# Kernel optimization log

Measured on AMD Instinct MI355X. Metric: run time of the kernel, lower is better.

## Reference

```python
import jax, jax.numpy as jnp
import numpy as np

H = 64

def _ln(x, g, b, eps=1e-5):
    m = x.mean(-1, keepdims=True)
    v = ((x - m) ** 2).mean(-1, keepdims=True)
    return (x - m) * jax.lax.rsqrt(v + eps) * g + b

def _sage(x_src, x_dst, src, dst, Wl, bl, Wr, n_dst):
    # PyG SAGEConv: mean-aggregate neighbors, lin_l(agg) + lin_r(x_dst)
    msg = x_src[src]  # [E, H] gather
    s = jax.ops.segment_sum(msg, dst, num_segments=n_dst)
    cnt = jax.ops.segment_sum(jnp.ones((src.shape[0], 1), x_src.dtype), dst, num_segments=n_dst)
    mean = s / jnp.maximum(cnt, 1.0)
    return mean @ Wl + bl + x_dst @ Wr

def _hetero_conv(xn, xc, edge_sim, men_src, men_dst, edge_rel, Wl, bl, Wr):
    # relation order: 0=similar_to (news->news), 1=mentions (news->company), 2=related_to (company->company)
    Nn, Nc = xn.shape[0], xc.shape[0]
    on = _sage(xn, xn, edge_sim[0], edge_sim[1], Wl[0], bl[0], Wr[0], Nn)
    oc = (_sage(xn, xc, men_src, men_dst, Wl[1], bl[1], Wr[1], Nc)
          + _sage(xc, xc, edge_rel[0], edge_rel[1], Wl[2], bl[2], Wr[2], Nc))  # HeteroConv aggr='sum'
    return on, oc

def setup_inputs():
    key = jax.random.key(0)
    ks = jax.random.split(key, 16)
    Nn, Nc = 100000, 5000
    Es, Em, Er = 3200000, 1000000, 160000
    init = lambda k, s: (jax.random.normal(k, s, jnp.float32) * 0.05)
    d = {}
    d['x_news'] = jax.random.normal(ks[0], (Nn, 385), jnp.float32)
    d['x_company'] = jax.random.normal(ks[1], (Nc, 24), jnp.float32)
    d['edge_sim'] = jax.random.randint(ks[2], (2, Es), 0, Nn)
    d['men_src'] = jax.random.randint(ks[3], (Em,), 0, Nn)
    d['men_dst'] = jax.random.randint(ks[4], (Em,), 0, Nc)
    d['edge_rel'] = jax.random.randint(ks[5], (2, Er), 0, Nc)
    d['nw_W'] = init(ks[6], (385, H)); d['nw_b'] = jnp.zeros((H,), jnp.float32)
    d['cw_W'] = init(ks[7], (24, H)); d['cw_b'] = jnp.zeros((H,), jnp.float32)
    d['n1n_g'] = jnp.ones((H,), jnp.float32); d['n1n_b'] = jnp.zeros((H,), jnp.float32)
    d['n1c_g'] = jnp.ones((H,), jnp.float32); d['n1c_b'] = jnp.zeros((H,), jnp.float32)
    d['c1_Wl'] = init(ks[8], (3, H, H)); d['c1_bl'] = jnp.zeros((3, H), jnp.float32)
    d['c1_Wr'] = init(ks[9], (3, H, H))
    d['c2_Wl'] = init(ks[10], (3, H, H)); d['c2_bl'] = jnp.zeros((3, H), jnp.float32)
    d['c2_Wr'] = init(ks[11], (3, H, H))
    d['cls_W1'] = init(ks[12], (H, 32)); d['cls_b1'] = jnp.zeros((32,), jnp.float32)
    d['cls_W2'] = init(ks[13], (32, 1)); d['cls_b2'] = jnp.zeros((1,), jnp.float32)
    return d

def reference(x_news, x_company, edge_sim, men_src, men_dst, edge_rel,
              nw_W, nw_b, cw_W, cw_b, n1n_g, n1n_b, n1c_g, n1c_b,
              c1_Wl, c1_bl, c1_Wr, c2_Wl, c2_bl, c2_Wr,
              cls_W1, cls_b1, cls_W2, cls_b2):
    xn0 = jax.nn.relu(x_news @ nw_W + nw_b)
    xc0 = jax.nn.relu(x_company @ cw_W + cw_b)
    on, oc = _hetero_conv(xn0, xc0, edge_sim, men_src, men_dst, edge_rel, c1_Wl, c1_bl, c1_Wr)
    xn = _ln(jax.nn.relu(on), n1n_g, n1n_b)
    xc = _ln(jax.nn.relu(oc + xc0), n1c_g, n1c_b)
    # dropout is identity in eval mode
    on2, oc2 = _hetero_conv(xn, xc, edge_sim, men_src, men_dst, edge_rel, c2_Wl, c2_bl, c2_Wr)
    comp = jax.nn.relu(oc2 + xc)  # [Nc, H]
    h = jax.nn.relu(comp @ cls_W1 + cls_b1)
    return (h @ cls_W2 + cls_b2).squeeze(-1)  # [Nc]
```

## Files before the change

### kernel.cpp

```cpp
#include <hip/hip_runtime.h>
#include <hip/hip_bf16.h>

#define HF 64

__global__ __launch_bounds__(256) void k_proj_news(
    const float* __restrict__ A, const float* __restrict__ W,
    const float* __restrict__ b, float* __restrict__ out, int M)
{
    __shared__ float As[16][68];
    __shared__ float Ws[16][64];
    const int t = threadIdx.x;
    const int r0 = blockIdx.x * 64;
    const int rt = t >> 4, ct = t & 15;
    float acc[4][4] = {};

    for (int c0 = 0; c0 < 385; c0 += 16) {
        int lr = t >> 2, lk0 = (t & 3) * 4;
        #pragma unroll
        for (int j = 0; j < 4; ++j) {
            int k = c0 + lk0 + j;
            float v = 0.f;
            if ((r0 + lr) < M && k < 385) v = A[(size_t)(r0 + lr) * 385 + k];
            As[lk0 + j][lr] = v;
        }
        #pragma unroll
        for (int j = 0; j < 4; ++j) {
            int idx = j * 256 + t;
            int k = idx >> 6, col = idx & 63;
            float v = 0.f;
            if (c0 + k < 385) v = W[(size_t)(c0 + k) * 64 + col];
            Ws[k][col] = v;
        }
        __syncthreads();
        #pragma unroll
        for (int kk = 0; kk < 16; ++kk) {
            float4 a = *(const float4*)&As[kk][rt * 4];
            float4 w = *(const float4*)&Ws[kk][ct * 4];
            float av[4] = {a.x, a.y, a.z, a.w};
            float wv[4] = {w.x, w.y, w.z, w.w};
            #pragma unroll
            for (int i = 0; i < 4; ++i)
                #pragma unroll
                for (int j = 0; j < 4; ++j)
                    acc[i][j] += av[i] * wv[j];
        }
        __syncthreads();
    }
    float4 bv = *(const float4*)&b[ct * 4];
    float bb[4] = {bv.x, bv.y, bv.z, bv.w};
    #pragma unroll
    for (int i = 0; i < 4; ++i) {
        int row = r0 + rt * 4 + i;
        if (row < M) {
            float4 o;
            o.x = fmaxf(acc[i][0] + bb[0], 0.f);
            o.y = fmaxf(acc[i][1] + bb[1], 0.f);
            o.z = fmaxf(acc[i][2] + bb[2], 0.f);
            o.w = fmaxf(acc[i][3] + bb[3], 0.f);
            *(float4*)&out[(size_t)row * HF + ct * 4] = o;
        }
    }
}

__global__ __launch_bounds__(256) void k_proj_comp(
    const float* __restrict__ A, const float* __restrict__ W,
    const float* __restrict__ b, float* __restrict__ out, int M)
{
    int idx = blockIdx.x * blockDim.x + threadIdx.x;
    if (idx >= M * HF) return;
    int row = idx >> 6, col = idx & 63;
    float acc = b[col];
    #pragma unroll
    for (int k = 0; k < 24; ++k)
        acc += A[(size_t)row * 24 + k] * W[k * HF + col];
    out[idx] = fmaxf(acc, 0.f);
}

__global__ void k_count(const int* __restrict__ dst, int n, int base,
                        unsigned* __restrict__ cnt)
{
    for (int i = blockIdx.x * blockDim.x + threadIdx.x; i < n;
         i += gridDim.x * blockDim.x)
        atomicAdd(&cnt[base + dst[i]], 1u);
}

__global__ __launch_bounds__(1024) void k_scan(
    const unsigned* __restrict__ cnt, int n,
    int* __restrict__ off, int* __restrict__ cursor)
{
    __shared__ int wsum[17];
    __shared__ int carry_s;
    if (threadIdx.x == 0) carry_s = 0;
    __syncthreads();
    const int lane = threadIdx.x & 63, wid = threadIdx.x >> 6;
    for (int base = 0; base < n; base += 1024) {
        int i = base + (int)threadIdx.x;
        int v = (i < n) ? (int)cnt[i] : 0;
        int x = v;
        #pragma unroll
        for (int s = 1; s < 64; s <<= 1) {
            int t = __shfl_up(x, s, 64);
            if (lane >= s) x += t;
        }
        if (lane == 63) wsum[wid] = x;
        __syncthreads();
        if (threadIdx.x == 0) {
            int run = 0;
            #pragma unroll
            for (int w = 0; w < 16; ++w) { int t = wsum[w]; wsum[w] = run; run += t; }
            wsum[16] = run;
        }
        __syncthreads();
        int excl = x - v + wsum[wid] + carry_s;
        if (i < n) { off[i] = excl; cursor[i] = excl; }
        __syncthreads();
        if (threadIdx.x == 0) carry_s += wsum[16];
        __syncthreads();
    }
    if (threadIdx.x == 0) off[n] = carry_s;
}

__global__ void k_fill(const int* __restrict__ src, const int* __restrict__ dst,
                       int n, int dbase, int* __restrict__ cursor,
                       int* __restrict__ bucket)
{
    for (int i = blockIdx.x * blockDim.x + threadIdx.x; i < n;
         i += gridDim.x * blockDim.x) {
        int pos = atomicAdd(&cursor[dbase + dst[i]], 1);
        bucket[pos] = src[i];
    }
}

__global__ __launch_bounds__(256) void k_gather(
    const int* __restrict__ off, const int* __restrict__ bucket,
    const float* __restrict__ x, float* __restrict__ out, int obase, int M)
{
    const int lane = threadIdx.x & 63;
    const int w = (int)((blockIdx.x * blockDim.x + threadIdx.x) >> 6);
    if (w >= M) return;
    int o0 = off[obase + w], o1 = off[obase + w + 1];
    float a0 = 0.f, a1 = 0.f, a2 = 0.f, a3 = 0.f;
    int e = o0;
    for (; e + 4 <= o1; e += 4) {
        int s0 = bucket[e], s1 = bucket[e + 1], s2 = bucket[e + 2], s3 = bucket[e + 3];
        a0 += x[(size_t)s0 * HF + lane];
        a1 += x[(size_t)s1 * HF + lane];
        a2 += x[(size_t)s2 * HF + lane];
        a3 += x[(size_t)s3 * HF + lane];
    }
    for (; e < o1; ++e) a0 += x[(size_t)bucket[e] * HF + lane];
    float acc = (a0 + a1) + (a2 + a3);
    float inv = 1.f / fmaxf((float)(o1 - o0), 1.f);
    out[(size_t)w * HF + lane] = acc * inv;
}

__global__ __launch_bounds__(256) void k_news_l1(
    const float* __restrict__ mean_sim, const float* __restrict__ xn0,
    const float* __restrict__ Wl, const float* __restrict__ bl,
    const float* __restrict__ Wr,
    const float* __restrict__ g, const float* __restrict__ be,
    float* __restrict__ xn, int M)
{
    __shared__ float A1[64][68];
    __shared__ float A2[64][68];
    const int t = threadIdx.x;
    const int r0 = blockIdx.x * 64;
    const int lrow = t & 63;
    const int wq = t >> 6;

    bool rok = (r0 + lrow) < M;
    #pragma unroll
    for (int j4 = 0; j4 < 4; ++j4) {
        int k0 = wq * 16 + j4 * 4;
        float4 v1 = make_float4(0.f, 0.f, 0.f, 0.f), v2 = v1;
        if (rok) {
            v1 = *(const float4*)&mean_sim[(size_t)(r0 + lrow) * HF + k0];
            v2 = *(const float4*)&xn0[(size_t)(r0 + lrow) * HF + k0];
        }
        A1[k0 + 0][lrow] = v1.x; A1[k0 + 1][lrow] = v1.y;
        A1[k0 + 2][lrow] = v1.z; A1[k0 + 3][lrow] = v1.w;
        A2[k0 + 0][lrow] = v2.x; A2[k0 + 1][lrow] = v2.y;
        A2[k0 + 2][lrow] = v2.z; A2[k0 + 3][lrow] = v2.w;
    }
    __syncthreads();

    const int rt = t >> 4, ct = t & 15;
    float acc[4][4] = {};
    #pragma unroll 16
    for (int kk = 0; kk < 64; ++kk) {
        float4 a1 = *(const float4*)&A1[kk][rt * 4];
        float4 a2 = *(const float4*)&A2[kk][rt * 4];
        float4 wl = *(const float4*)&Wl[(size_t)kk * HF + ct * 4];
        float4 wr = *(const float4*)&Wr[(size_t)kk * HF + ct * 4];
        float a1v[4] = {a1.x, a1.y, a1.z, a1.w};
        float a2v[4] = {a2.x, a2.y, a2.z, a2.w};
        float wlv[4] = {wl.x, wl.y, wl.z, wl.w};
        float wrv[4] = {wr.x, wr.y, wr.z, wr.w};
        #pragma unroll
        for (int i = 0; i < 4; ++i)
            #pragma unroll
            for (int j = 0; j < 4; ++j)
                acc[i][j] += a1v[i] * wlv[j] + a2v[i] * wrv[j];
    }
    __syncthreads();
    float (*C)[68] = A1;
    float4 blv = *(const float4*)&bl[ct * 4];
    float blb[4] = {blv.x, blv.y, blv.z, blv.w};
    #pragma unroll
    for (int i = 0; i < 4; ++i) {
        float4 o;
        o.x = fmaxf(acc[i][0] + blb[0], 0.f);
        o.y = fmaxf(acc[i][1] + blb[1], 0.f);
        o.z = fmaxf(acc[i][2] + blb[2], 0.f);
        o.w = fmaxf(acc[i][3] + blb[3], 0.f);
        *(float4*)&C[rt * 4 + i][ct * 4] = o;
    }
    __syncthreads();

    const int lane = t & 63, wid = t >> 6;
    float gl = g[lane], bel = be[lane];
    for (int rr = 0; rr < 16; ++rr) {
        int row = wid * 16 + rr;
        float v = C[row][lane];
        float s = v, q = v * v;
        #pragma unroll
        for (int m = 1; m < 64; m <<= 1) {
            s += __shfl_xor(s, m, 64);
            q += __shfl_xor(q, m, 64);
        }
        float mean = s * (1.f / 64.f);
        float var = q * (1.f / 64.f) - mean * mean;
        float r = rsqrtf(var + 1e-5f);
        int grow = r0 + row;
        if (grow < M) xn[(size_t)grow * HF + lane] = (v - mean) * r * gl + bel;
    }
}

__global__ __launch_bounds__(256) void k_comp_l1(
    const float* __restrict__ mean_men, const float* __restrict__ mean_rel,
    const float* __restrict__ xc0,
    const float* __restrict__ Wl1, const float* __restrict__ bl1,
    const float* __restrict__ Wr1,
    const float* __restrict__ Wl2, const float* __restrict__ bl2,
    const float* __restrict__ Wr2,
    const float* __restrict__ g, const float* __restrict__ be,
    float* __restrict__ xc, int M)
{
    const int lane = threadIdx.x & 63;
    const int node = (int)((blockIdx.x * blockDim.x + threadIdx.x) >> 6);
    if (node >= M) return;
    float mm = mean_men[(size_t)node * HF + lane];
    float mr = mean_rel[(size_t)node * HF + lane];
    float xv = xc0[(size_t)node * HF + lane];
    float acc = bl1[lane] + bl2[lane];
    #pragma unroll 8
    for (int k = 0; k < 64; ++k) {
        float amm = __shfl(mm, k, 64);
        float amr = __shfl(mr, k, 64);
        float ax  = __shfl(xv, k, 64);
        acc += amm * Wl1[k * HF + lane] + ax * Wr1[k * HF + lane]
             + amr * Wl2[k * HF + lane] + ax * Wr2[k * HF + lane];
    }
    float pre = fmaxf(acc + xv, 0.f);
    float s = pre, q = pre * pre;
    #pragma unroll
    for (int m = 1; m < 64; m <<= 1) {
        s += __shfl_xor(s, m, 64);
        q += __shfl_xor(q, m, 64);
    }
    float mean = s * (1.f / 64.f);
    float var = q * (1.f / 64.f) - mean * mean;
    float r = rsqrtf(var + 1e-5f);
    xc[(size_t)node * HF + lane] = (pre - mean) * r * g[lane] + be[lane];
}

__global__ __launch_bounds__(256) void k_final(
    const float* __restrict__ mean_men, const float* __restrict__ mean_rel,
    const float* __restrict__ xc,
    const float* __restrict__ Wl1, const float* __restrict__ bl1,
    const float* __restrict__ Wr1,
    const float* __restrict__ Wl2, const float* __restrict__ bl2,
    const float* __restrict__ Wr2,
    const float* __restrict__ W1, const float* __restrict__ b1,
    const float* __restrict__ W2, const float* __restrict__ b2,
    float* __restrict__ out, int M)
{
    const int lane = threadIdx.x & 63;
    const int node = (int)((blockIdx.x * blockDim.x + threadIdx.x) >> 6);
    if (node >= M) return;
    float mm = mean_men[(size_t)node * HF + lane];
    float mr = mean_rel[(size_t)node * HF + lane];
    float xv = xc[(size_t)node * HF + lane];
    float acc = bl1[lane] + bl2[lane];
    #pragma unroll 8
    for (int k = 0; k < 64; ++k) {
        float amm = __shfl(mm, k, 64);
        float amr = __shfl(mr, k, 64);
        float ax  = __shfl(xv, k, 64);
        acc += amm * Wl1[k * HF + lane] + ax * (Wr1[k * HF + lane] + Wr2[k * HF + lane])
             + amr * Wl2[k * HF + lane];
    }
    float comp = fmaxf(acc + xv, 0.f);
    const int l31 = lane & 31;
    float hacc = b1[l31];
    #pragma unroll 8
    for (int j = 0; j < 64; ++j) {
        float cj = __shfl(comp, j, 64);
        hacc += cj * W1[j * 32 + l31];
    }
    float h = fmaxf(hacc, 0.f);
    float p = (lane < 32) ? h * W2[l31] : 0.f;
    #pragma unroll
    for (int m = 16; m >= 1; m >>= 1) p += __shfl_xor(p, m, 64);
    if (lane == 0) out[node] = p + b2[0];
}

extern "C" void kernel_launch(void* const* d_in, const int* in_sizes, int n_in,
                              void* d_out, int out_size, void* d_ws, size_t ws_size,
                              hipStream_t stream)
{
    const float* x_news  = (const float*)d_in[0];
    const float* x_comp  = (const float*)d_in[1];
    const int*   edge_sim = (const int*)d_in[2];
    const int*   men_src  = (const int*)d_in[3];
    const int*   men_dst  = (const int*)d_in[4];
    const int*   edge_rel = (const int*)d_in[5];
    const float* nw_W = (const float*)d_in[6];
    const float* nw_b = (const float*)d_in[7];
    const float* cw_W = (const float*)d_in[8];
    const float* cw_b = (const float*)d_in[9];
    const float* n1n_g = (const float*)d_in[10];
    const float* n1n_b = (const float*)d_in[11];
    const float* n1c_g = (const float*)d_in[12];
    const float* n1c_b = (const float*)d_in[13];
    const float* c1_Wl = (const float*)d_in[14];
    const float* c1_bl = (const float*)d_in[15];
    const float* c1_Wr = (const float*)d_in[16];
    const float* c2_Wl = (const float*)d_in[17];
    const float* c2_bl = (const float*)d_in[18];
    const float* c2_Wr = (const float*)d_in[19];
    const float* cls_W1 = (const float*)d_in[20];
    const float* cls_b1 = (const float*)d_in[21];
    const float* cls_W2 = (const float*)d_in[22];
    const float* cls_b2 = (const float*)d_in[23];

    const int Nn = in_sizes[0] / 385;
    const int Nc = in_sizes[1] / 24;
    const int Es = in_sizes[2] / 2;
    const int Em = in_sizes[3];
    const int Er = in_sizes[5] / 2;
    const int* sim_src = edge_sim;
    const int* sim_dst = edge_sim + Es;
    const int* rel_src = edge_rel;
    const int* rel_dst = edge_rel + Er;
    const int ND = Nn + 2 * Nc;
    const int E  = Es + Em + Er;

    float* ws = (float*)d_ws;
    size_t o = 0;
    unsigned* cnt = (unsigned*)(ws + o); o += ND;
    int* off    = (int*)(ws + o); o += ND + 1;
    int* cursor = (int*)(ws + o); o += ND;
    int* bucket = (int*)(ws + o); o += E;
    float* mean_sim = ws + o; o += (size_t)Nn * HF;
    float* mean_men1 = ws + o; o += (size_t)Nc * HF;
    float* mean_rel1 = ws + o; o += (size_t)Nc * HF;
    float* xn0 = ws + o; o += (size_t)Nn * HF;
    float* xn  = ws + o; o += (size_t)Nn * HF;
    float* xc0 = ws + o; o += (size_t)Nc * HF;
    float* xc  = ws + o; o += (size_t)Nc * HF;
    float* mean_men2 = mean_sim;
    float* mean_rel2 = mean_sim + (size_t)Nc * HF;

    hipMemsetAsync(cnt, 0, (size_t)ND * sizeof(unsigned), stream);

    k_proj_news<<<(Nn + 63) / 64, 256, 0, stream>>>(x_news, nw_W, nw_b, xn0, Nn);
    k_proj_comp<<<(Nc * HF + 255) / 256, 256, 0, stream>>>(x_comp, cw_W, cw_b, xc0, Nc);

    k_count<<<1024, 256, 0, stream>>>(sim_dst, Es, 0, cnt);
    k_count<<<512, 256, 0, stream>>>(men_dst, Em, Nn, cnt);
    k_count<<<256, 256, 0, stream>>>(rel_dst, Er, Nn + Nc, cnt);
    k_scan<<<1, 1024, 0, stream>>>(cnt, ND, off, cursor);
    k_fill<<<1024, 256, 0, stream>>>(sim_src, sim_dst, Es, 0, cursor, bucket);
    k_fill<<<512, 256, 0, stream>>>(men_src, men_dst, Em, Nn, cursor, bucket);
    k_fill<<<256, 256, 0, stream>>>(rel_src, rel_dst, Er, Nn + Nc, cursor, bucket);

    k_gather<<<(Nn + 3) / 4, 256, 0, stream>>>(off, bucket, xn0, mean_sim, 0, Nn);
    k_gather<<<(Nc + 3) / 4, 256, 0, stream>>>(off, bucket, xn0, mean_men1, Nn, Nc);
    k_gather<<<(Nc + 3) / 4, 256, 0, stream>>>(off, bucket, xc0, mean_rel1, Nn + Nc, Nc);

    k_news_l1<<<(Nn + 63) / 64, 256, 0, stream>>>(
        mean_sim, xn0, c1_Wl, c1_bl, c1_Wr, n1n_g, n1n_b, xn, Nn);
    k_comp_l1<<<(Nc * HF + 255) / 256, 256, 0, stream>>>(
        mean_men1, mean_rel1, xc0,
        c1_Wl + 4096, c1_bl + 64, c1_Wr + 4096,
        c1_Wl + 8192, c1_bl + 128, c1_Wr + 8192,
        n1c_g, n1c_b, xc, Nc);

    k_gather<<<(Nc + 3) / 4, 256, 0, stream>>>(off, bucket, xn, mean_men2, Nn, Nc);
    k_gather<<<(Nc + 3) / 4, 256, 0, stream>>>(off, bucket, xc, mean_rel2, Nn + Nc, Nc);

    k_final<<<(Nc * HF + 255) / 256, 256, 0, stream>>>(
        mean_men2, mean_rel2, xc,
        c2_Wl + 4096, c2_bl + 64, c2_Wr + 4096,
        c2_Wl + 8192, c2_bl + 128, c2_Wr + 8192,
        cls_W1, cls_b1, cls_W2, cls_b2, (float*)d_out, Nc);
}
```

Baseline: 1.506 ms.

## Replace full CSR build for similar_to edges with coarse binning and LDS aggregation

For the 3.2M news->news edges, the per-destination CSR fill is replaced by a coarse partition into bins of 256 destinations. Each entry packs the source index with the low 8 bits of the destination. Each bin is then aggregated by one 512-thread block that accumulates rows in LDS with shared atomics. The aim is to cut the scattered global atomics and writes of the per-node fill and the uncoalesced gather pass. In exchange it adds a bin histogram and scan, needs 64KB of LDS per block, and packs source indices into 17 bits, which assumes fewer than 131072 news nodes.

```diff
diff --git a/kernel.cpp b/kernel.cpp
--- a/kernel.cpp
+++ b/kernel.cpp
@@ -2,6 +2,9 @@
 #include <hip/hip_bf16.h>
 
 #define HF 64
+#define BINSZ 256
+#define NBIN_S 392
+#define PCHUNK 4096
 
 __global__ __launch_bounds__(256) void k_proj_news(
     const float* __restrict__ A, const float* __restrict__ W,
@@ -84,6 +87,20 @@
         atomicAdd(&cnt[base + dst[i]], 1u);
 }
 
+__global__ __launch_bounds__(256) void k_binhist(
+    const int* __restrict__ dst, int n, unsigned* __restrict__ bins)
+{
+    __shared__ unsigned h[NBIN_S];
+    for (int i = threadIdx.x; i < NBIN_S; i += 256) h[i] = 0;
+    __syncthreads();
+    for (int i = blockIdx.x * blockDim.x + threadIdx.x; i < n;
+         i += gridDim.x * blockDim.x)
+        atomicAdd(&h[dst[i] >> 8], 1u);
+    __syncthreads();
+    for (int i = threadIdx.x; i < NBIN_S; i += 256)
+        if (h[i]) atomicAdd(&bins[i], h[i]);
+}
+
 __global__ __launch_bounds__(1024) void k_scan(
     const unsigned* __restrict__ cnt, int n,
     int* __restrict__ off, int* __restrict__ cursor)
@@ -118,6 +135,76 @@
         __syncthreads();
     }
     if (threadIdx.x == 0) off[n] = carry_s;
+}
+
+__global__ __launch_bounds__(256) void k_partition(
+    const int* __restrict__ src, const int* __restrict__ dst, int n,
+    int* __restrict__ cursor, unsigned* __restrict__ binned)
+{
+    __shared__ unsigned stage[PCHUNK];
+    __shared__ int hist[NBIN_S];
+    __shared__ int rank[NBIN_S];
+    __shared__ int base[NBIN_S];
+    for (long long c0 = (long long)blockIdx.x * PCHUNK; c0 < n;
+         c0 += (long long)gridDim.x * PCHUNK) {
+        int nc = min((long long)PCHUNK, (long long)n - c0);
+        for (int i = threadIdx.x; i < NBIN_S; i += 256) { hist[i] = 0; rank[i] = 0; }
+        __syncthreads();
+        for (int i = threadIdx.x; i < nc; i += 256) {
+            int d = dst[c0 + i];
+            stage[i] = (unsigned)src[c0 + i] | ((unsigned)(d & 255) << 17);
+            atomicAdd(&hist[d >> 8], 1);
+        }
+        __syncthreads();
+        for (int i = threadIdx.x; i < NBIN_S; i += 256)
+            if (hist[i]) base[i] = atomicAdd(&cursor[i], hist[i]);
+        __syncthreads();
+        for (int i = threadIdx.x; i < nc; i += 256) {
+            int b = dst[c0 + i] >> 8;
+            int r = atomicAdd(&rank[b], 1);
+            binned[base[b] + r] = stage[i];
+        }
+        __syncthreads();
+    }
+}
+
+__global__ __launch_bounds__(512) void k_binagg(
+    const unsigned* __restrict__ binned, const int* __restrict__ bin_off,
+    const unsigned* __restrict__ cnt, const float* __restrict__ feat,
+    float* __restrict__ out, int M)
+{
+    __shared__ __align__(16) float acc[BINSZ * HF];
+    const int tid = threadIdx.x, lane = tid & 63, wv = tid >> 6;
+    for (int i = tid; i < BINSZ * HF / 4; i += 512)
+        ((float4*)acc)[i] = make_float4(0.f, 0.f, 0.f, 0.f);
+    __syncthreads();
+    const int b = blockIdx.x;
+    const int e0 = bin_off[b], e1 = bin_off[b + 1];
+    for (int eb = e0 + wv * 4; eb < e1; eb += 32) {
+        unsigned p0 = 0, p1 = 0, p2 = 0, p3 = 0;
+        int m = e1 - eb;
+        p0 = binned[eb];
+        if (m > 1) p1 = binned[eb + 1];
+        if (m > 2) p2 = binned[eb + 2];
+        if (m > 3) p3 = binned[eb + 3];
+        float v0 = feat[(size_t)(p0 & 0x1FFFF) * HF + lane];
+        float v1 = (m > 1) ? feat[(size_t)(p1 & 0x1FFFF) * HF + lane] : 0.f;
+        float v2 = (m > 2) ? feat[(size_t)(p2 & 0x1FFFF) * HF + lane] : 0.f;
+        float v3 = (m > 3) ? feat[(size_t)(p3 & 0x1FFFF) * HF + lane] : 0.f;
+        atomicAdd(&acc[(p0 >> 17) * HF + lane], v0);
+        if (m > 1) atomicAdd(&acc[(p1 >> 17) * HF + lane], v1);
+        if (m > 2) atomicAdd(&acc[(p2 >> 17) * HF + lane], v2);
+        if (m > 3) atomicAdd(&acc[(p3 >> 17) * HF + lane], v3);
+    }
+    __syncthreads();
+    const int d0 = b * BINSZ;
+    for (int r = wv; r < BINSZ; r += 8) {
+        int row = d0 + r;
+        if (row < M) {
+            float inv = 1.f / fmaxf((float)cnt[row], 1.f);
+            out[(size_t)row * HF + lane] = acc[r * HF + lane] * inv;
+        }
+    }
 }
 
 __global__ void k_fill(const int* __restrict__ src, const int* __restrict__ dst,
@@ -353,16 +440,21 @@
     const int* sim_dst = edge_sim + Es;
     const int* rel_src = edge_rel;
     const int* rel_dst = edge_rel + Er;
-    const int ND = Nn + 2 * Nc;
-    const int E  = Es + Em + Er;
+    const int NDc = 2 * Nc;
 
     float* ws = (float*)d_ws;
     size_t o = 0;
-    unsigned* cnt = (unsigned*)(ws + o); o += ND;
-    int* off    = (int*)(ws + o); o += ND + 1;
-    int* cursor = (int*)(ws + o); o += ND;
-    int* bucket = (int*)(ws + o); o += E;
-    float* mean_sim = ws + o; o += (size_t)Nn * HF;
+    unsigned* cnt_sim = (unsigned*)(ws + o); o += Nn;
+    unsigned* cnt_c   = (unsigned*)(ws + o); o += NDc;
+    unsigned* binh    = (unsigned*)(ws + o); o += NBIN_S;
+    const size_t zero_bytes = o * sizeof(float);
+    int* bin_off = (int*)(ws + o); o += NBIN_S + 1;
+    int* bin_cur = (int*)(ws + o); o += NBIN_S;
+    int* off_c   = (int*)(ws + o); o += NDc + 1;
+    int* cur_c   = (int*)(ws + o); o += NDc;
+    unsigned* binned_sim = (unsigned*)(ws + o); o += Es;
+    int* bucket_c = (int*)(ws + o); o += Em + Er;
+    float* mean_sim  = ws + o; o += (size_t)Nn * HF;
     float* mean_men1 = ws + o; o += (size_t)Nc * HF;
     float* mean_rel1 = ws + o; o += (size_t)Nc * HF;
     float* xn0 = ws + o; o += (size_t)Nn * HF;
@@ -372,22 +464,25 @@
     float* mean_men2 = mean_sim;
     float* mean_rel2 = mean_sim + (size_t)Nc * HF;
 
-    hipMemsetAsync(cnt, 0, (size_t)ND * sizeof(unsigned), stream);
+    hipMemsetAsync(ws, 0, zero_bytes, stream);
 
     k_proj_news<<<(Nn + 63) / 64, 256, 0, stream>>>(x_news, nw_W, nw_b, xn0, Nn);
     k_proj_comp<<<(Nc * HF + 255) / 256, 256, 0, stream>>>(x_comp, cw_W, cw_b, xc0, Nc);
 
-    k_count<<<1024, 256, 0, stream>>>(sim_dst, Es, 0, cnt);
-    k_count<<<512, 256, 0, stream>>>(men_dst, Em, Nn, cnt);
-    k_count<<<256, 256, 0, stream>>>(rel_dst, Er, Nn + Nc, cnt);
-    k_scan<<<1, 1024, 0, stream>>>(cnt, ND, off, cursor);
-    k_fill<<<1024, 256, 0, stream>>>(sim_src, sim_dst, Es, 0, cursor, bucket);
-    k_fill<<<512, 256, 0, stream>>>(men_src, men_dst, Em, Nn, cursor, bucket);
-    k_fill<<<256, 256, 0, stream>>>(rel_src, rel_dst, Er, Nn + Nc, cursor, bucket);
-
-    k_gather<<<(Nn + 3) / 4, 256, 0, stream>>>(off, bucket, xn0, mean_sim, 0, Nn);
-    k_gather<<<(Nc + 3) / 4, 256, 0, stream>>>(off, bucket, xn0, mean_men1, Nn, Nc);
-    k_gather<<<(Nc + 3) / 4, 256, 0, stream>>>(off, bucket, xc0, mean_rel1, Nn + Nc, Nc);
+    k_count<<<1024, 256, 0, stream>>>(sim_dst, Es, 0, cnt_sim);
+    k_binhist<<<512, 256, 0, stream>>>(sim_dst, Es, binh);
+    k_scan<<<1, 1024, 0, stream>>>(binh, NBIN_S, bin_off, bin_cur);
+    k_partition<<<512, 256, 0, stream>>>(sim_src, sim_dst, Es, bin_cur, binned_sim);
+
+    k_count<<<512, 256, 0, stream>>>(men_dst, Em, 0, cnt_c);
+    k_count<<<256, 256, 0, stream>>>(rel_dst, Er, Nc, cnt_c);
+    k_scan<<<1, 1024, 0, stream>>>(cnt_c, NDc, off_c, cur_c);
+    k_fill<<<512, 256, 0, stream>>>(men_src, men_dst, Em, 0, cur_c, bucket_c);
+    k_fill<<<256, 256, 0, stream>>>(rel_src, rel_dst, Er, Nc, cur_c, bucket_c);
+
+    k_binagg<<<NBIN_S, 512, 0, stream>>>(binned_sim, bin_off, cnt_sim, xn0, mean_sim, Nn);
+    k_gather<<<(Nc + 3) / 4, 256, 0, stream>>>(off_c, bucket_c, xn0, mean_men1, 0, Nc);
+    k_gather<<<(Nc + 3) / 4, 256, 0, stream>>>(off_c, bucket_c, xc0, mean_rel1, Nc, Nc);
 
     k_news_l1<<<(Nn + 63) / 64, 256, 0, stream>>>(
         mean_sim, xn0, c1_Wl, c1_bl, c1_Wr, n1n_g, n1n_b, xn, Nn);
@@ -397,8 +492,8 @@
         c1_Wl + 8192, c1_bl + 128, c1_Wr + 8192,
         n1c_g, n1c_b, xc, Nc);
 
-    k_gather<<<(Nc + 3) / 4, 256, 0, stream>>>(off, bucket, xn, mean_men2, Nn, Nc);
-    k_gather<<<(Nc + 3) / 4, 256, 0, stream>>>(off, bucket, xc, mean_rel2, Nn + Nc, Nc);
+    k_gather<<<(Nc + 3) / 4, 256, 0, stream>>>(off_c, bucket_c, xn, mean_men2, 0, Nc);
+    k_gather<<<(Nc + 3) / 4, 256, 0, stream>>>(off_c, bucket_c, xc, mean_rel2, Nc, Nc);
 
     k_final<<<(Nc * HF + 255) / 256, 256, 0, stream>>>(
         mean_men2, mean_rel2, xc,
```

Measured after the change: 2.403 ms. +59.6%, slower.

## Replace CSR gather with bf16 atomic scatter-add edge aggregation

Applied to the files above, without the earlier changes.

Removes the scan, fill and CSR bucket build. Neighbour sums are instead computed by scattering each edge's source features into fp32 destination sums with atomics, and are normalized later by precomputed inverse degree counts. Node features used in aggregation are stored as bf16 to halve gather traffic. This costs precision in the aggregated features and adds heavy float atomic contention, especially on the 5000 company nodes receiving a million mention edges.

```diff
diff --git a/kernel.cpp b/kernel.cpp
--- a/kernel.cpp
+++ b/kernel.cpp
@@ -3,9 +3,19 @@
 
 #define HF 64
 
+__device__ __forceinline__ unsigned short f2b(float f) {
+    unsigned u = __float_as_uint(f);
+    u += 0x7FFFu + ((u >> 16) & 1u);
+    return (unsigned short)(u >> 16);
+}
+__device__ __forceinline__ float b2f(unsigned short b) {
+    return __uint_as_float((unsigned)b << 16);
+}
+
 __global__ __launch_bounds__(256) void k_proj_news(
     const float* __restrict__ A, const float* __restrict__ W,
-    const float* __restrict__ b, float* __restrict__ out, int M)
+    const float* __restrict__ b, float* __restrict__ out,
+    unsigned short* __restrict__ outb, int M)
 {
     __shared__ float As[16][68];
     __shared__ float Ws[16][64];
@@ -58,13 +68,17 @@
             o.z = fmaxf(acc[i][2] + bb[2], 0.f);
             o.w = fmaxf(acc[i][3] + bb[3], 0.f);
             *(float4*)&out[(size_t)row * HF + ct * 4] = o;
+            ushort4 ob;
+            ob.x = f2b(o.x); ob.y = f2b(o.y); ob.z = f2b(o.z); ob.w = f2b(o.w);
+            *(ushort4*)&outb[(size_t)row * HF + ct * 4] = ob;
         }
     }
 }
 
 __global__ __launch_bounds__(256) void k_proj_comp(
     const float* __restrict__ A, const float* __restrict__ W,
-    const float* __restrict__ b, float* __restrict__ out, int M)
+    const float* __restrict__ b, float* __restrict__ out,
+    unsigned short* __restrict__ outb, int M)
 {
     int idx = blockIdx.x * blockDim.x + threadIdx.x;
     if (idx >= M * HF) return;
@@ -73,7 +87,9 @@
     #pragma unroll
     for (int k = 0; k < 24; ++k)
         acc += A[(size_t)row * 24 + k] * W[k * HF + col];
-    out[idx] = fmaxf(acc, 0.f);
+    float o = fmaxf(acc, 0.f);
+    out[idx] = o;
+    outb[idx] = f2b(o);
 }
 
 __global__ void k_count(const int* __restrict__ dst, int n, int base,
@@ -84,82 +100,38 @@
         atomicAdd(&cnt[base + dst[i]], 1u);
 }
 
-__global__ __launch_bounds__(1024) void k_scan(
-    const unsigned* __restrict__ cnt, int n,
-    int* __restrict__ off, int* __restrict__ cursor)
-{
-    __shared__ int wsum[17];
-    __shared__ int carry_s;
-    if (threadIdx.x == 0) carry_s = 0;
-    __syncthreads();
-    const int lane = threadIdx.x & 63, wid = threadIdx.x >> 6;
-    for (int base = 0; base < n; base += 1024) {
-        int i = base + (int)threadIdx.x;
-        int v = (i < n) ? (int)cnt[i] : 0;
-        int x = v;
-        #pragma unroll
-        for (int s = 1; s < 64; s <<= 1) {
-            int t = __shfl_up(x, s, 64);
-            if (lane >= s) x += t;
-        }
-        if (lane == 63) wsum[wid] = x;
-        __syncthreads();
-        if (threadIdx.x == 0) {
-            int run = 0;
-            #pragma unroll
-            for (int w = 0; w < 16; ++w) { int t = wsum[w]; wsum[w] = run; run += t; }
-            wsum[16] = run;
-        }
-        __syncthreads();
-        int excl = x - v + wsum[wid] + carry_s;
-        if (i < n) { off[i] = excl; cursor[i] = excl; }
-        __syncthreads();
-        if (threadIdx.x == 0) carry_s += wsum[16];
-        __syncthreads();
-    }
-    if (threadIdx.x == 0) off[n] = carry_s;
-}
-
-__global__ void k_fill(const int* __restrict__ src, const int* __restrict__ dst,
-                       int n, int dbase, int* __restrict__ cursor,
-                       int* __restrict__ bucket)
-{
-    for (int i = blockIdx.x * blockDim.x + threadIdx.x; i < n;
-         i += gridDim.x * blockDim.x) {
-        int pos = atomicAdd(&cursor[dbase + dst[i]], 1);
-        bucket[pos] = src[i];
-    }
-}
-
-__global__ __launch_bounds__(256) void k_gather(
-    const int* __restrict__ off, const int* __restrict__ bucket,
-    const float* __restrict__ x, float* __restrict__ out, int obase, int M)
+__global__ void k_inv(const unsigned* __restrict__ cnt, float* __restrict__ inv, int n)
+{
+    int i = blockIdx.x * blockDim.x + threadIdx.x;
+    if (i < n) inv[i] = 1.0f / fmaxf((float)cnt[i], 1.0f);
+}
+
+__global__ __launch_bounds__(256) void k_aggb(
+    const int* __restrict__ src, const int* __restrict__ dst,
+    const unsigned short* __restrict__ x, float* __restrict__ sum, int n)
 {
     const int lane = threadIdx.x & 63;
-    const int w = (int)((blockIdx.x * blockDim.x + threadIdx.x) >> 6);
-    if (w >= M) return;
-    int o0 = off[obase + w], o1 = off[obase + w + 1];
-    float a0 = 0.f, a1 = 0.f, a2 = 0.f, a3 = 0.f;
-    int e = o0;
-    for (; e + 4 <= o1; e += 4) {
-        int s0 = bucket[e], s1 = bucket[e + 1], s2 = bucket[e + 2], s3 = bucket[e + 3];
-        a0 += x[(size_t)s0 * HF + lane];
-        a1 += x[(size_t)s1 * HF + lane];
-        a2 += x[(size_t)s2 * HF + lane];
-        a3 += x[(size_t)s3 * HF + lane];
-    }
-    for (; e < o1; ++e) a0 += x[(size_t)bucket[e] * HF + lane];
-    float acc = (a0 + a1) + (a2 + a3);
-    float inv = 1.f / fmaxf((float)(o1 - o0), 1.f);
-    out[(size_t)w * HF + lane] = acc * inv;
+    int w = (blockIdx.x * blockDim.x + threadIdx.x) >> 6;
+    const int nw = (gridDim.x * blockDim.x) >> 6;
+    for (int e = w * 2; e < n; e += nw * 2) {
+        int s0 = src[e], d0 = dst[e];
+        bool h1 = (e + 1) < n;
+        int s1 = h1 ? src[e + 1] : 0;
+        int d1 = h1 ? dst[e + 1] : 0;
+        float v0 = b2f(x[(size_t)s0 * HF + lane]);
+        float v1 = h1 ? b2f(x[(size_t)s1 * HF + lane]) : 0.f;
+        atomicAdd(&sum[(size_t)d0 * HF + lane], v0);
+        if (h1) atomicAdd(&sum[(size_t)d1 * HF + lane], v1);
+    }
 }
 
 __global__ __launch_bounds__(256) void k_news_l1(
-    const float* __restrict__ mean_sim, const float* __restrict__ xn0,
+    const float* __restrict__ sum_sim, const float* __restrict__ invc,
+    const float* __restrict__ xn0,
     const float* __restrict__ Wl, const float* __restrict__ bl,
     const float* __restrict__ Wr,
     const float* __restrict__ g, const float* __restrict__ be,
-    float* __restrict__ xn, int M)
+    unsigned short* __restrict__ xnb, int M)
 {
     __shared__ float A1[64][68];
     __shared__ float A2[64][68];
@@ -169,16 +141,17 @@
     const int wq = t >> 6;
 
     bool rok = (r0 + lrow) < M;
+    float invr = rok ? invc[r0 + lrow] : 0.f;
     #pragma unroll
     for (int j4 = 0; j4 < 4; ++j4) {
         int k0 = wq * 16 + j4 * 4;
         float4 v1 = make_float4(0.f, 0.f, 0.f, 0.f), v2 = v1;
         if (rok) {
-            v1 = *(const float4*)&mean_sim[(size_t)(r0 + lrow) * HF + k0];
+            v1 = *(const float4*)&sum_sim[(size_t)(r0 + lrow) * HF + k0];
             v2 = *(const float4*)&xn0[(size_t)(r0 + lrow) * HF + k0];
         }
-        A1[k0 + 0][lrow] = v1.x; A1[k0 + 1][lrow] = v1.y;
-        A1[k0 + 2][lrow] = v1.z; A1[k0 + 3][lrow] = v1.w;
+        A1[k0 + 0][lrow] = v1.x * invr; A1[k0 + 1][lrow] = v1.y * invr;
+        A1[k0 + 2][lrow] = v1.z * invr; A1[k0 + 3][lrow] = v1.w * invr;
         A2[k0 + 0][lrow] = v2.x; A2[k0 + 1][lrow] = v2.y;
         A2[k0 + 2][lrow] = v2.z; A2[k0 + 3][lrow] = v2.w;
     }
@@ -232,25 +205,27 @@
         float var = q * (1.f / 64.f) - mean * mean;
         float r = rsqrtf(var + 1e-5f);
         int grow = r0 + row;
-        if (grow < M) xn[(size_t)grow * HF + lane] = (v - mean) * r * gl + bel;
+        if (grow < M)
+            xnb[(size_t)grow * HF + lane] = f2b((v - mean) * r * gl + bel);
     }
 }
 
 __global__ __launch_bounds__(256) void k_comp_l1(
-    const float* __restrict__ mean_men, const float* __restrict__ mean_rel,
+    const float* __restrict__ sum_men, const float* __restrict__ inv_men,
+    const float* __restrict__ sum_rel, const float* __restrict__ inv_rel,
     const float* __restrict__ xc0,
     const float* __restrict__ Wl1, const float* __restrict__ bl1,
     const float* __restrict__ Wr1,
     const float* __restrict__ Wl2, const float* __restrict__ bl2,
     const float* __restrict__ Wr2,
     const float* __restrict__ g, const float* __restrict__ be,
-    float* __restrict__ xc, int M)
+    float* __restrict__ xc, unsigned short* __restrict__ xcb, int M)
 {
     const int lane = threadIdx.x & 63;
     const int node = (int)((blockIdx.x * blockDim.x + threadIdx.x) >> 6);
     if (node >= M) return;
-    float mm = mean_men[(size_t)node * HF + lane];
-    float mr = mean_rel[(size_t)node * HF + lane];
+    float mm = sum_men[(size_t)node * HF + lane] * inv_men[node];
+    float mr = sum_rel[(size_t)node * HF + lane] * inv_rel[node];
     float xv = xc0[(size_t)node * HF + lane];
     float acc = bl1[lane] + bl2[lane];
     #pragma unroll 8
@@ -271,11 +246,14 @@
     float mean = s * (1.f / 64.f);
     float var = q * (1.f / 64.f) - mean * mean;
     float r = rsqrtf(var + 1e-5f);
-    xc[(size_t)node * HF + lane] = (pre - mean) * r * g[lane] + be[lane];
+    float o = (pre - mean) * r * g[lane] + be[lane];
+    xc[(size_t)node * HF + lane] = o;
+    xcb[(size_t)node * HF + lane] = f2b(o);
 }
 
 __global__ __launch_bounds__(256) void k_final(
-    const float* __restrict__ mean_men, const float* __restrict__ mean_rel,
+    const float* __restrict__ sum_men, const float* __restrict__ inv_men,
+    const float* __restrict__ sum_rel, const float* __restrict__ inv_rel,
     const float* __restrict__ xc,
     const float* __restrict__ Wl1, const float* __restrict__ bl1,
     const float* __restrict__ Wr1,
@@ -288,8 +266,8 @@
     const int lane = threadIdx.x & 63;
     const int node = (int)((blockIdx.x * blockDim.x + threadIdx.x) >> 6);
     if (node >= M) return;
-    float mm = mean_men[(size_t)node * HF + lane];
-    float mr = mean_rel[(size_t)node * HF + lane];
+    float mm = sum_men[(size_t)node * HF + lane] * inv_men[node];
+    float mr = sum_rel[(size_t)node * HF + lane] * inv_rel[node];
     float xv = xc[(size_t)node * HF + lane];
     float acc = bl1[lane] + bl2[lane];
     #pragma unroll 8
@@ -353,55 +331,56 @@
     const int* sim_dst = edge_sim + Es;
     const int* rel_src = edge_rel;
     const int* rel_dst = edge_rel + Er;
-    const int ND = Nn + 2 * Nc;
-    const int E  = Es + Em + Er;
 
     float* ws = (float*)d_ws;
     size_t o = 0;
-    unsigned* cnt = (unsigned*)(ws + o); o += ND;
-    int* off    = (int*)(ws + o); o += ND + 1;
-    int* cursor = (int*)(ws + o); o += ND;
-    int* bucket = (int*)(ws + o); o += E;
-    float* mean_sim = ws + o; o += (size_t)Nn * HF;
-    float* mean_men1 = ws + o; o += (size_t)Nc * HF;
-    float* mean_rel1 = ws + o; o += (size_t)Nc * HF;
+    float* sum_sim  = ws + o; o += (size_t)Nn * HF;
+    float* sum_men1 = ws + o; o += (size_t)Nc * HF;
+    float* sum_rel1 = ws + o; o += (size_t)Nc * HF;
+    float* sum_men2 = ws + o; o += (size_t)Nc * HF;
+    float* sum_rel2 = ws + o; o += (size_t)Nc * HF;
+    unsigned* cnt_all = (unsigned*)(ws + o); o += (size_t)Nn + 2 * Nc;
+    const size_t zero_bytes = o * sizeof(float);
+    float* inv_all = ws + o; o += (size_t)Nn + 2 * Nc;
     float* xn0 = ws + o; o += (size_t)Nn * HF;
-    float* xn  = ws + o; o += (size_t)Nn * HF;
     float* xc0 = ws + o; o += (size_t)Nc * HF;
     float* xc  = ws + o; o += (size_t)Nc * HF;
-    float* mean_men2 = mean_sim;
-    float* mean_rel2 = mean_sim + (size_t)Nc * HF;
-
-    hipMemsetAsync(cnt, 0, (size_t)ND * sizeof(unsigned), stream);
-
-    k_proj_news<<<(Nn + 63) / 64, 256, 0, stream>>>(x_news, nw_W, nw_b, xn0, Nn);
-    k_proj_comp<<<(Nc * HF + 255) / 256, 256, 0, stream>>>(x_comp, cw_W, cw_b, xc0, Nc);
-
-    k_count<<<1024, 256, 0, stream>>>(sim_dst, Es, 0, cnt);
-    k_count<<<512, 256, 0, stream>>>(men_dst, Em, Nn, cnt);
-    k_count<<<256, 256, 0, stream>>>(rel_dst, Er, Nn + Nc, cnt);
-    k_scan<<<1, 1024, 0, stream>>>(cnt, ND, off, cursor);
-    k_fill<<<1024, 256, 0, stream>>>(sim_src, sim_dst, Es, 0, cursor, bucket);
-    k_fill<<<512, 256, 0, stream>>>(men_src, men_dst, Em, Nn, cursor, bucket);
-    k_fill<<<256, 256, 0, stream>>>(rel_src, rel_dst, Er, Nn + Nc, cursor, bucket);
-
-    k_gather<<<(Nn + 3) / 4, 256, 0, stream>>>(off, bucket, xn0, mean_sim, 0, Nn);
-    k_gather<<<(Nc + 3) / 4, 256, 0, stream>>>(off, bucket, xn0, mean_men1, Nn, Nc);
-    k_gather<<<(Nc + 3) / 4, 256, 0, stream>>>(off, bucket, xc0, mean_rel1, Nn + Nc, Nc);
+    unsigned short* xn0b = (unsigned short*)(ws + o); o += (size_t)Nn * HF / 2;
+    unsigned short* xnb  = (unsigned short*)(ws + o); o += (size_t)Nn * HF / 2;
+    unsigned short* xc0b = (unsigned short*)(ws + o); o += (size_t)Nc * HF / 2;
+    unsigned short* xcb  = (unsigned short*)(ws + o); o += (size_t)Nc * HF / 2;
+
+    float* inv_sim = inv_all;
+    float* inv_men = inv_all + Nn;
+    float* inv_rel = inv_all + Nn + Nc;
+
+    hipMemsetAsync(d_ws, 0, zero_bytes, stream);
+
+    k_proj_news<<<(Nn + 63) / 64, 256, 0, stream>>>(x_news, nw_W, nw_b, xn0, xn0b, Nn);
+    k_proj_comp<<<(Nc * HF + 255) / 256, 256, 0, stream>>>(x_comp, cw_W, cw_b, xc0, xc0b, Nc);
+
+    k_count<<<1024, 256, 0, stream>>>(sim_dst, Es, 0, cnt_all);
+    k_count<<<512, 256, 0, stream>>>(men_dst, Em, Nn, cnt_all);
+    k_count<<<256, 256, 0, stream>>>(rel_dst, Er, Nn + Nc, cnt_all);
+    k_inv<<<(Nn + 2 * Nc + 255) / 256, 256, 0, stream>>>(cnt_all, inv_all, Nn + 2 * Nc);
+
+    k_aggb<<<2048, 256, 0, stream>>>(sim_src, sim_dst, xn0b, sum_sim, Es);
+    k_aggb<<<1024, 256, 0, stream>>>(men_src, men_dst, xn0b, sum_men1, Em);
+    k_aggb<<<256, 256, 0, stream>>>(rel_src, rel_dst, xc0b, sum_rel1, Er);
 
     k_news_l1<<<(Nn + 63) / 64, 256, 0, stream>>>(
-        mean_sim, xn0, c1_Wl, c1_bl, c1_Wr, n1n_g, n1n_b, xn, Nn);
+        sum_sim, inv_sim, xn0, c1_Wl, c1_bl, c1_Wr, n1n_g, n1n_b, xnb, Nn);
     k_comp_l1<<<(Nc * HF + 255) / 256, 256, 0, stream>>>(
-        mean_men1, mean_rel1, xc0,
+        sum_men1, inv_men, sum_rel1, inv_rel, xc0,
         c1_Wl + 4096, c1_bl + 64, c1_Wr + 4096,
         c1_Wl + 8192, c1_bl + 128, c1_Wr + 8192,
-        n1c_g, n1c_b, xc, Nc);
-
-    k_gather<<<(Nc + 3) / 4, 256, 0, stream>>>(off, bucket, xn, mean_men2, Nn, Nc);
-    k_gather<<<(Nc + 3) / 4, 256, 0, stream>>>(off, bucket, xc, mean_rel2, Nn + Nc, Nc);
+        n1c_g, n1c_b, xc, xcb, Nc);
+
+    k_aggb<<<1024, 256, 0, stream>>>(men_src, men_dst, xnb, sum_men2, Em);
+    k_aggb<<<256, 256, 0, stream>>>(rel_src, rel_dst, xcb, sum_rel2, Er);
 
     k_final<<<(Nc * HF + 255) / 256, 256, 0, stream>>>(
-        mean_men2, mean_rel2, xc,
+        sum_men2, inv_men, sum_rel2, inv_rel, xc,
         c2_Wl + 4096, c2_bl + 64, c2_Wr + 4096,
         c2_Wl + 8192, c2_bl + 128, c2_Wr + 8192,
         cls_W1, cls_b1, cls_W2, cls_b2, (float*)d_out, Nc);
```

After: 2.030 ms. 1.35x slower.
